# Optimization experiments

Measured on AMD Instinct MI355X. Metric: run time of the kernel, lower is better.

Reference implementation:

```python
import jax, jax.numpy as jnp
import numpy as np

B, T, D, H, L = 32, 512, 1024, 1024, 2


def setup_inputs() -> dict:
    key = jax.random.key(0)
    ks = jax.random.split(key, 7)
    s_in = 1.0 / np.sqrt(D)
    s_h = 1.0 / np.sqrt(H)
    return {
        "x": jax.random.normal(ks[0], (B, T, D), dtype=jnp.float32),
        # layer 0: input_size = D
        "W_ih0": jax.random.uniform(ks[1], (4 * H, D), jnp.float32, -s_in, s_in),
        "b0": jax.random.uniform(ks[2], (4 * H,), jnp.float32, -s_in, s_in),
        "W_hh0": jax.random.uniform(ks[3], (4 * H, H), jnp.float32, -s_h, s_h),
        # layer 1: input_size = H
        "W_ih1": jax.random.uniform(ks[4], (4 * H, H), jnp.float32, -s_h, s_h),
        "b1": jax.random.uniform(ks[5], (4 * H,), jnp.float32, -s_h, s_h),
        "W_hh1": jax.random.uniform(ks[6], (4 * H, H), jnp.float32, -s_h, s_h),
    }


def _lstm_layer(x_seq, W_ih, b, W_hh):
    # x_seq: [T, B, Din]. Precompute the input-to-gate GEMM for all steps
    # (mathematically identical to per-step, but one big GEMM).
    gx = jnp.einsum('tbd,gd->tbg', x_seq, W_ih) + b  # [T, B, 4H]
    h0 = jnp.zeros((x_seq.shape[1], W_hh.shape[1]), x_seq.dtype)
    c0 = jnp.zeros_like(h0)

    def step(carry, gx_t):
        h, c = carry
        gates = gx_t + h @ W_hh.T  # [B, 4H]
        i, f, g, o = jnp.split(gates, 4, axis=-1)  # torch chunk order: i,f,g,o
        i = jax.nn.sigmoid(i)
        f = jax.nn.sigmoid(f)
        g = jnp.tanh(g)
        o = jax.nn.sigmoid(o)
        c_new = f * c + i * g
        h_new = o * jnp.tanh(c_new)
        return (h_new, c_new), h_new

    (h_n, c_n), hs = jax.lax.scan(step, (h0, c0), gx)
    return hs, h_n, c_n  # hs: [T, B, H]


def reference(x, W_ih0, b0, W_hh0, W_ih1, b1, W_hh1):
    xs = jnp.transpose(x, (1, 0, 2))  # batch_first -> [T, B, D]
    hs0, h0_n, c0_n = _lstm_layer(xs, W_ih0, b0, W_hh0)
    hs1, h1_n, c1_n = _lstm_layer(hs0, W_ih1, b1, W_hh1)
    output = jnp.transpose(hs1, (1, 0, 2))  # [B, T, H]
    h_n = jnp.stack([h0_n, h1_n], axis=0)  # [L, B, H]
    c_n = jnp.stack([c0_n, c1_n], axis=0)
    return output, (h_n, c_n)
```

## Files before the change

### kernel.cpp

```cpp
#include <hip/hip_runtime.h>
#include <stdint.h>

typedef __attribute__((ext_vector_type(8))) short short8;
typedef __attribute__((ext_vector_type(4))) short short4v;
typedef __attribute__((ext_vector_type(4))) float f32x4;
typedef __attribute__((ext_vector_type(4))) unsigned int u32x4;
typedef __attribute__((ext_vector_type(4))) int i32x4;
typedef __attribute__((ext_vector_type(2))) unsigned long long u64x2;

__device__ inline unsigned short f2bf(float f) {
  unsigned int u = __builtin_bit_cast(unsigned int, f);
  u += 0x7fffu + ((u >> 16) & 1u);
  return (unsigned short)(u >> 16);
}
__device__ inline float bf2f(unsigned short s) {
  return __builtin_bit_cast(float, (unsigned int)s << 16);
}

__device__ inline unsigned long long stale64(unsigned long long v) {
  unsigned long long x = v ^ 0x7f7f7f7f7f7f7f7full;
  return (x - 0x0001000100010001ull) & ~x & 0x8000800080008000ull;
}


__global__ __launch_bounds__(256) void cvt_x_kernel(const float* __restrict__ x,
                                                    short* __restrict__ xbf) {
  const int total = (16384 * 1024) / 4;
  for (int i = blockIdx.x * blockDim.x + threadIdx.x; i < total;
       i += gridDim.x * blockDim.x) {
    int d4 = i & 255;
    int m  = i >> 8;
    int t = m >> 5, b = m & 31;
    float4 v = *(const float4*)(x + ((size_t)b * 512 + t) * 1024 + (size_t)d4 * 4);
    short4v o;
    o.x = (short)f2bf(v.x); o.y = (short)f2bf(v.y);
    o.z = (short)f2bf(v.z); o.w = (short)f2bf(v.w);
    *(short4v*)(xbf + (size_t)m * 1024 + d4 * 4) = o;
  }
}

__global__ __launch_bounds__(256) void cvt_w_kernel(const float* __restrict__ W,
                                                    short* __restrict__ Wp) {
  const int total = (4096 * 1024) / 4;
  for (int i = blockIdx.x * blockDim.x + threadIdx.x; i < total;
       i += gridDim.x * blockDim.x) {
    int k4 = i & 255;
    int n  = i >> 8;
    int g = n & 3, j = n >> 2;
    float4 v = *(const float4*)(W + ((size_t)g * 1024 + j) * 1024 + (size_t)k4 * 4);
    short4v o;
    o.x = (short)f2bf(v.x); o.y = (short)f2bf(v.y);
    o.z = (short)f2bf(v.z); o.w = (short)f2bf(v.w);
    *(short4v*)(Wp + (size_t)n * 1024 + k4 * 4) = o;
  }
}

__global__ __launch_bounds__(256) void cvt_b_kernel(const float* __restrict__ b,
                                                    float* __restrict__ bp) {
  int n = blockIdx.x * blockDim.x + threadIdx.x;
  if (n < 4096) bp[n] = b[(n & 3) * 1024 + (n >> 2)];
}

__global__ __launch_bounds__(256) void gemm_bt(const short* __restrict__ A,
                                               const short* __restrict__ Bm,
                                               short* __restrict__ C) {
  const int n0 = blockIdx.x * 128;
  const int m0 = blockIdx.y * 128;
  const int tid = threadIdx.x;
  const int lane = tid & 63, wid = tid >> 6;
  const int wr = wid >> 1, wc = wid & 1;
  const int fr = lane & 15, fq = lane >> 4;

  __shared__ __align__(16) short As[128 * 32];
  __shared__ __align__(16) short Bs[128 * 32];

  f32x4 acc[4][4];
#pragma unroll
  for (int i = 0; i < 4; i++)
#pragma unroll
    for (int j = 0; j < 4; j++) acc[i][j] = (f32x4){0.f, 0.f, 0.f, 0.f};

  for (int kt = 0; kt < 1024; kt += 32) {
#pragma unroll
    for (int s = 0; s < 2; s++) {
      int c = tid + s * 256;
      int row = c >> 2;
      int off = (c & 3) * 8;
      *(u32x4*)&As[row * 32 + off] =
          *(const u32x4*)(A + (size_t)(n0 + row) * 1024 + kt + off);
      *(u32x4*)&Bs[row * 32 + off] =
          *(const u32x4*)(Bm + (size_t)(m0 + row) * 1024 + kt + off);
    }
    __syncthreads();
    short8 af[4], bf[4];
#pragma unroll
    for (int i = 0; i < 4; i++)
      af[i] = *(const short8*)&As[(wr * 64 + i * 16 + fr) * 32 + fq * 8];
#pragma unroll
    for (int j = 0; j < 4; j++)
      bf[j] = *(const short8*)&Bs[(wc * 64 + j * 16 + fr) * 32 + fq * 8];
#pragma unroll
    for (int i = 0; i < 4; i++)
#pragma unroll
      for (int j = 0; j < 4; j++)
        acc[i][j] = __builtin_amdgcn_mfma_f32_16x16x32_bf16(af[i], bf[j], acc[i][j], 0, 0, 0);
    __syncthreads();
  }

#pragma unroll
  for (int i = 0; i < 4; i++) {
#pragma unroll
    for (int j = 0; j < 4; j++) {
      int nq = n0 + wr * 64 + i * 16 + fq * 4;
      int m = m0 + wc * 64 + j * 16 + fr;
      int t = m >> 5, b = m & 31;
      unsigned long long pk = 0;
#pragma unroll
      for (int r = 0; r < 4; r++)
        pk |= (unsigned long long)f2bf(acc[i][j][r]) << (16 * r);
      *(unsigned long long*)&C[(size_t)t * 131072 + (size_t)b * 4096 + nq] = pk;
    }
  }
}

#define POLL8(HBP)                                                            \
  do {                                                                        \
    i32x4 r0, r1, r2, r3, r4, r5, r6, r7;                                     \
    while (true) {                                                            \
      asm volatile(                                                           \
          "global_load_dwordx4 %0, %8, %16 sc0 sc1\n\t"                       \
          "global_load_dwordx4 %1, %9, %16 sc0 sc1\n\t"                       \
          "global_load_dwordx4 %2, %10, %16 sc0 sc1\n\t"                      \
          "global_load_dwordx4 %3, %11, %16 sc0 sc1\n\t"                      \
          "global_load_dwordx4 %4, %12, %16 sc0 sc1\n\t"                      \
          "global_load_dwordx4 %5, %13, %16 sc0 sc1\n\t"                      \
          "global_load_dwordx4 %6, %14, %16 sc0 sc1\n\t"                      \
          "global_load_dwordx4 %7, %15, %16 sc0 sc1\n\t"                      \
          "s_waitcnt vmcnt(0)"                                                \
          : "=&v"(r0), "=&v"(r1), "=&v"(r2), "=&v"(r3), "=&v"(r4),            \
            "=&v"(r5), "=&v"(r6), "=&v"(r7)                                   \
          : "v"(soff[0]), "v"(soff[1]), "v"(soff[2]), "v"(soff[3]),           \
            "v"(soff[4]), "v"(soff[5]), "v"(soff[6]), "v"(soff[7]),           \
            "s"(HBP)                                                          \
          : "memory");                                                        \
      u64x2 q0 = __builtin_bit_cast(u64x2, r0), q1 = __builtin_bit_cast(u64x2, r1); \
      u64x2 q2 = __builtin_bit_cast(u64x2, r2), q3 = __builtin_bit_cast(u64x2, r3); \
      u64x2 q4 = __builtin_bit_cast(u64x2, r4), q5 = __builtin_bit_cast(u64x2, r5); \
      u64x2 q6 = __builtin_bit_cast(u64x2, r6), q7 = __builtin_bit_cast(u64x2, r7); \
      unsigned long long bad =                                                \
          stale64(q0.x) | stale64(q0.y) | stale64(q1.x) | stale64(q1.y) |     \
          stale64(q2.x) | stale64(q2.y) | stale64(q3.x) | stale64(q3.y) |     \
          stale64(q4.x) | stale64(q4.y) | stale64(q5.x) | stale64(q5.y) |     \
          stale64(q6.x) | stale64(q6.y) | stale64(q7.x) | stale64(q7.y);      \
      if (!bad) break;                                                        \
    }                                                                         \
    *(i32x4*)&img[widx[0]] = r0;                                              \
    *(i32x4*)&img[widx[1]] = r1;                                              \
    *(i32x4*)&img[widx[2]] = r2;                                              \
    *(i32x4*)&img[widx[3]] = r3;                                              \
    *(i32x4*)&img[widx[4]] = r4;                                              \
    *(i32x4*)&img[widx[5]] = r5;                                              \
    *(i32x4*)&img[widx[6]] = r6;                                              \
    *(i32x4*)&img[widx[7]] = r7;                                              \
  } while (0)

__global__ __launch_bounds__(512, 1) void lstm_fused(
    const short* __restrict__ gx0, const short* __restrict__ whh0,
    const float* __restrict__ b0p, const short* __restrict__ wih1,
    const short* __restrict__ whh1, const float* __restrict__ b1p,
    short* __restrict__ hs0, short* __restrict__ hs1,
    float* __restrict__ out, float* __restrict__ hn, float* __restrict__ cn) {
  const int tid = threadIdx.x;
  const int lane = tid & 63, w = tid >> 6;
  const int fr = lane & 15, fq = lane >> 4;

  __shared__ __align__(16) short img[32 * 1024];
  __shared__ __align__(16) float red[4 * 64 * 4];

  if (blockIdx.x < 64) {
    const int rg = (int)blockIdx.x >> 1, bg = (int)blockIdx.x & 1;
    const int n_base = rg * 128 + w * 16;
    const int b = bg * 16 + fr;
    const int jb = rg * 32 + w * 4;
    const int j = jb + fq;
    const int sw = fr & 7;

    const short* arow = whh0 + (size_t)(n_base + fr) * 1024 + fq * 8;
    short8 wreg[32];
#pragma unroll
    for (int kk = 0; kk < 32; kk++) wreg[kk] = *(const short8*)(arow + kk * 32);

    float bia[4];
#pragma unroll
    for (int r = 0; r < 4; r++) bia[r] = b0p[n_base + fq * 4 + r];

    unsigned int soff[4];
    int widx[4];
#pragma unroll
    for (int i = 0; i < 4; i++) {
      int ch = tid + i * 512;
      soff[i] = (unsigned int)ch * 16;
      int bb = ch >> 7, cc = ch & 127;
      widx[i] = bb * 1024 + ((cc ^ (bb & 7)) << 3);
    }

    float cell = 0.f;
    for (int t = 0; t < 512; ++t) {
      unsigned long long gq = *(const unsigned long long*)(
          gx0 + (size_t)t * 131072 + (size_t)b * 4096 + n_base + fq * 4);

      if (t > 0) {
        const short* hbp = hs0 + (size_t)(t - 1) * 32768 + bg * 16384;
        i32x4 r0, r1, r2, r3;
        while (true) {
          asm volatile(
              "global_load_dwordx4 %0, %4, %8 sc0 sc1\n\t"
              "global_load_dwordx4 %1, %5, %8 sc0 sc1\n\t"
              "global_load_dwordx4 %2, %6, %8 sc0 sc1\n\t"
              "global_load_dwordx4 %3, %7, %8 sc0 sc1\n\t"
              "s_waitcnt vmcnt(0)"
              : "=&v"(r0), "=&v"(r1), "=&v"(r2), "=&v"(r3)
              : "v"(soff[0]), "v"(soff[1]), "v"(soff[2]), "v"(soff[3]),
                "s"(hbp)
              : "memory");
          u64x2 q0 = __builtin_bit_cast(u64x2, r0);
          u64x2 q1 = __builtin_bit_cast(u64x2, r1);
          u64x2 q2 = __builtin_bit_cast(u64x2, r2);
          u64x2 q3 = __builtin_bit_cast(u64x2, r3);
          unsigned long long bad =
              stale64(q0.x) | stale64(q0.y) | stale64(q1.x) | stale64(q1.y) |
              stale64(q2.x) | stale64(q2.y) | stale64(q3.x) | stale64(q3.y);
          if (!bad) break;
        }
        *(i32x4*)&img[widx[0]] = r0;
        *(i32x4*)&img[widx[1]] = r1;
        *(i32x4*)&img[widx[2]] = r2;
        *(i32x4*)&img[widx[3]] = r3;
      }
      __syncthreads();

      f32x4 a0 = (f32x4){0.f,0.f,0.f,0.f}, a1 = (f32x4){0.f,0.f,0.f,0.f};
      f32x4 a2 = (f32x4){0.f,0.f,0.f,0.f}, a3 = (f32x4){0.f,0.f,0.f,0.f};
      if (t > 0) {
#pragma unroll
        for (int m = 0; m < 8; m++) {
          const int chb = fq + m * 16;
          short8 bv0 = *(const short8*)&img[fr * 1024 + (((chb + 0) ^ sw) << 3)];
          short8 bv1 = *(const short8*)&img[fr * 1024 + (((chb + 4) ^ sw) << 3)];
          short8 bv2 = *(const short8*)&img[fr * 1024 + (((chb + 8) ^ sw) << 3)];
          short8 bv3 = *(const short8*)&img[fr * 1024 + (((chb + 12) ^ sw) << 3)];
          a0 = __builtin_amdgcn_mfma_f32_16x16x32_bf16(wreg[4 * m + 0], bv0, a0, 0, 0, 0);
          a1 = __builtin_amdgcn_mfma_f32_16x16x32_bf16(wreg[4 * m + 1], bv1, a1, 0, 0, 0);
          a2 = __builtin_amdgcn_mfma_f32_16x16x32_bf16(wreg[4 * m + 2], bv2, a2, 0, 0, 0);
          a3 = __builtin_amdgcn_mfma_f32_16x16x32_bf16(wreg[4 * m + 3], bv3, a3, 0, 0, 0);
        }
      }

      float pre0 = (a0[0] + a1[0]) + (a2[0] + a3[0]) + bf2f((unsigned short)(gq & 0xFFFF)) + bia[0];
      float pre1 = (a0[1] + a1[1]) + (a2[1] + a3[1]) + bf2f((unsigned short)((gq >> 16) & 0xFFFF)) + bia[1];
      float pre2 = (a0[2] + a1[2]) + (a2[2] + a3[2]) + bf2f((unsigned short)((gq >> 32) & 0xFFFF)) + bia[2];
      float pre3 = (a0[3] + a1[3]) + (a2[3] + a3[3]) + bf2f((unsigned short)((gq >> 48) & 0xFFFF)) + bia[3];

      float iv = 1.f / (1.f + __expf(-pre0));
      float fv = 1.f / (1.f + __expf(-pre1));
      float gv = 2.f / (1.f + __expf(-2.f * pre2)) - 1.f;
      float ov = 1.f / (1.f + __expf(-pre3));
      cell = fv * cell + iv * gv;
      float h = ov * (2.f / (1.f + __expf(-2.f * cell)) - 1.f);

      unsigned int hu = (unsigned int)f2bf(h);
      unsigned int v1 = __shfl(hu, fr + 16);
      unsigned int v2 = __shfl(hu, fr + 32);
      unsigned int v3 = __shfl(hu, fr + 48);
      if (fq == 0) {
        unsigned long long pk = (unsigned long long)hu |
                                ((unsigned long long)v1 << 16) |
                                ((unsigned long long)v2 << 32) |
                                ((unsigned long long)v3 << 48);
        __hip_atomic_store(
            (unsigned long long*)(hs0 + (size_t)t * 32768 + (size_t)b * 1024 + jb),
            pk, __ATOMIC_RELAXED, __HIP_MEMORY_SCOPE_AGENT);
      }
      if (t == 511) {
        hn[b * 1024 + j] = h;
        cn[b * 1024 + j] = cell;
        break;
      }
      __syncthreads();
    }
  } else {
    const int idx = (int)blockIdx.x - 64;
    const int rg = idx >> 1, bg = idx & 1;
    const int wn = w & 3, mw = w >> 2;
    const int n_base = rg * 64 + wn * 16;
    const int b = bg * 16 + fr;
    const int jb = rg * 16 + wn * 4;
    const int j = jb + fq;
    const int sw = fr & 7;
    const int ib = mw << 14;

    const short* wsrc = mw ? wih1 : whh1;
    const short* arow = wsrc + (size_t)(n_base + fr) * 1024 + fq * 8;
    short8 wreg[32];
#pragma unroll
    for (int kk = 0; kk < 32; kk++) wreg[kk] = *(const short8*)(arow + kk * 32);

    float bia[4];
#pragma unroll
    for (int r = 0; r < 4; r++) bia[r] = b1p[n_base + fq * 4 + r];

    const int lt = tid & 255;
    unsigned int soff[8];
    int widx[8];
#pragma unroll
    for (int i = 0; i < 8; i++) {
      int ch = lt + i * 256;
      soff[i] = (unsigned int)ch * 16;
      int bb = ch >> 7, cc = ch & 127;
      widx[i] = ib + bb * 1024 + ((cc ^ (bb & 7)) << 3);
    }

    float cell = 0.f;
    for (int t = 0; t < 512; ++t) {
      if (mw) {
        const short* hbp = hs0 + (size_t)t * 32768 + bg * 16384;
        POLL8(hbp);
      } else if (t > 0) {
        const short* hbp = hs1 + (size_t)(t - 1) * 32768 + bg * 16384;
        POLL8(hbp);
      }
      __syncthreads();

      f32x4 a0 = (f32x4){0.f,0.f,0.f,0.f}, a1 = (f32x4){0.f,0.f,0.f,0.f};
      f32x4 a2 = (f32x4){0.f,0.f,0.f,0.f}, a3 = (f32x4){0.f,0.f,0.f,0.f};
      if (mw || t > 0) {
#pragma unroll
        for (int m = 0; m < 8; m++) {
          const int chb = fq + m * 16;
          short8 bv0 = *(const short8*)&img[ib + fr * 1024 + (((chb + 0) ^ sw) << 3)];
          short8 bv1 = *(const short8*)&img[ib + fr * 1024 + (((chb + 4) ^ sw) << 3)];
          short8 bv2 = *(const short8*)&img[ib + fr * 1024 + (((chb + 8) ^ sw) << 3)];
          short8 bv3 = *(const short8*)&img[ib + fr * 1024 + (((chb + 12) ^ sw) << 3)];
          a0 = __builtin_amdgcn_mfma_f32_16x16x32_bf16(wreg[4 * m + 0], bv0, a0, 0, 0, 0);
          a1 = __builtin_amdgcn_mfma_f32_16x16x32_bf16(wreg[4 * m + 1], bv1, a1, 0, 0, 0);
          a2 = __builtin_amdgcn_mfma_f32_16x16x32_bf16(wreg[4 * m + 2], bv2, a2, 0, 0, 0);
          a3 = __builtin_amdgcn_mfma_f32_16x16x32_bf16(wreg[4 * m + 3], bv3, a3, 0, 0, 0);
        }
      }
      f32x4 s4 = (a0 + a1) + (a2 + a3);
      if (mw) *(f32x4*)&red[(wn * 64 + lane) * 4] = s4;
      __syncthreads();

      if (!mw) {
        const f32x4 o4 = *(const f32x4*)&red[(wn * 64 + lane) * 4];
        float pre0 = s4[0] + o4[0] + bia[0];
        float pre1 = s4[1] + o4[1] + bia[1];
        float pre2 = s4[2] + o4[2] + bia[2];
        float pre3 = s4[3] + o4[3] + bia[3];

        float iv = 1.f / (1.f + __expf(-pre0));
        float fv = 1.f / (1.f + __expf(-pre1));
        float gv = 2.f / (1.f + __expf(-2.f * pre2)) - 1.f;
        float ov = 1.f / (1.f + __expf(-pre3));
        cell = fv * cell + iv * gv;
        float h = ov * (2.f / (1.f + __expf(-2.f * cell)) - 1.f);

        unsigned int hu = (unsigned int)f2bf(h);
        unsigned int v1 = __shfl(hu, fr + 16);
        unsigned int v2 = __shfl(hu, fr + 32);
        unsigned int v3 = __shfl(hu, fr + 48);
        if (fq == 0) {
          unsigned long long pk = (unsigned long long)hu |
                                  ((unsigned long long)v1 << 16) |
                                  ((unsigned long long)v2 << 32) |
                                  ((unsigned long long)v3 << 48);
          __hip_atomic_store(
              (unsigned long long*)(hs1 + (size_t)t * 32768 + (size_t)b * 1024 + jb),
              pk, __ATOMIC_RELAXED, __HIP_MEMORY_SCOPE_AGENT);
        }
        out[(size_t)b * 524288 + (size_t)t * 1024 + j] = h;
        if (t == 511) {
          hn[32768 + b * 1024 + j] = h;
          cn[32768 + b * 1024 + j] = cell;
        }
      }
      if (t == 511) break;
      __syncthreads();
    }
  }
}

extern "C" void kernel_launch(void* const* d_in, const int* in_sizes, int n_in,
                              void* d_out, int out_size, void* d_ws, size_t ws_size,
                              hipStream_t stream) {
  const float* x    = (const float*)d_in[0];
  const float* Wih0 = (const float*)d_in[1];
  const float* b0   = (const float*)d_in[2];
  const float* Whh0 = (const float*)d_in[3];
  const float* Wih1 = (const float*)d_in[4];
  const float* b1   = (const float*)d_in[5];
  const float* Whh1 = (const float*)d_in[6];

  float* out = (float*)d_out;
  float* hn  = out + 16777216;
  float* cn  = hn + 65536;

  char* ws = (char*)d_ws;
  size_t off = 0;
  auto carve = [&](size_t bytes) {
    char* p = ws + off;
    off += (bytes + 255) & ~(size_t)255;
    return p;
  };
  short* xbf   = (short*)carve(16384ull * 1024 * 2);
  short* wih0p = (short*)carve(4096ull * 1024 * 2);
  short* whh0p = (short*)carve(4096ull * 1024 * 2);
  short* wih1p = (short*)carve(4096ull * 1024 * 2);
  short* whh1p = (short*)carve(4096ull * 1024 * 2);
  float* b0p   = (float*)carve(4096 * 4);
  float* b1p   = (float*)carve(4096 * 4);
  short* gx    = (short*)carve(512ull * 4096 * 32 * 2);
  short* hs0   = (short*)carve(16384ull * 1024 * 2);

  hipLaunchKernelGGL(cvt_x_kernel, dim3(4096), dim3(256), 0, stream, x, xbf);
  hipLaunchKernelGGL(cvt_w_kernel, dim3(1024), dim3(256), 0, stream, Wih0, wih0p);
  hipLaunchKernelGGL(cvt_w_kernel, dim3(1024), dim3(256), 0, stream, Whh0, whh0p);
  hipLaunchKernelGGL(cvt_w_kernel, dim3(1024), dim3(256), 0, stream, Wih1, wih1p);
  hipLaunchKernelGGL(cvt_w_kernel, dim3(1024), dim3(256), 0, stream, Whh1, whh1p);
  hipLaunchKernelGGL(cvt_b_kernel, dim3(16), dim3(256), 0, stream, b0, b0p);
  hipLaunchKernelGGL(cvt_b_kernel, dim3(16), dim3(256), 0, stream, b1, b1p);
  hipMemsetAsync(hs0, 0x7F, 16384ull * 1024 * 2, stream);

  hipLaunchKernelGGL(gemm_bt, dim3(32, 128), dim3(256), 0, stream, wih0p, xbf, gx);

  short* hs1 = xbf;
  hipMemsetAsync(hs1, 0x7F, 16384ull * 1024 * 2, stream);

  hipLaunchKernelGGL(lstm_fused, dim3(192), dim3(512), 0, stream,
                     (const short*)gx, (const short*)whh0p, (const float*)b0p,
                     (const short*)wih1p, (const short*)whh1p, (const float*)b1p,
                     hs0, hs1, out, hn, cn);
}
```

Before: 2.119 ms.

## Replace sentinel polling on hidden states with per-step block flags

Producer blocks now drain their stores, barrier, and set a per-timestep per-block flag. Consumers spin on that small flag array before doing a single load of the hidden-state slice, instead of repeatedly reloading the whole slice and checking for 0x7F sentinel values. This removes the two large sentinel memsets and the repeated full-slice polling traffic. The cost is an extra vmcnt drain and barrier on each step, plus one more memory round trip for the flag. The gx loads and output stores also become nontemporal.

```diff
diff --git a/kernel.cpp b/kernel.cpp
--- a/kernel.cpp
+++ b/kernel.cpp
@@ -6,7 +6,6 @@
 typedef __attribute__((ext_vector_type(4))) float f32x4;
 typedef __attribute__((ext_vector_type(4))) unsigned int u32x4;
 typedef __attribute__((ext_vector_type(4))) int i32x4;
-typedef __attribute__((ext_vector_type(2))) unsigned long long u64x2;
 
 __device__ inline unsigned short f2bf(float f) {
   unsigned int u = __builtin_bit_cast(unsigned int, f);
@@ -15,11 +14,6 @@
 }
 __device__ inline float bf2f(unsigned short s) {
   return __builtin_bit_cast(float, (unsigned int)s << 16);
-}
-
-__device__ inline unsigned long long stale64(unsigned long long v) {
-  unsigned long long x = v ^ 0x7f7f7f7f7f7f7f7full;
-  return (x - 0x0001000100010001ull) & ~x & 0x8000800080008000ull;
 }
 
 
@@ -123,37 +117,25 @@
   }
 }
 
-#define POLL8(HBP)                                                            \
+#define LOAD8(HBP)                                                            \
   do {                                                                        \
     i32x4 r0, r1, r2, r3, r4, r5, r6, r7;                                     \
-    while (true) {                                                            \
-      asm volatile(                                                           \
-          "global_load_dwordx4 %0, %8, %16 sc0 sc1\n\t"                       \
-          "global_load_dwordx4 %1, %9, %16 sc0 sc1\n\t"                       \
-          "global_load_dwordx4 %2, %10, %16 sc0 sc1\n\t"                      \
-          "global_load_dwordx4 %3, %11, %16 sc0 sc1\n\t"                      \
-          "global_load_dwordx4 %4, %12, %16 sc0 sc1\n\t"                      \
-          "global_load_dwordx4 %5, %13, %16 sc0 sc1\n\t"                      \
-          "global_load_dwordx4 %6, %14, %16 sc0 sc1\n\t"                      \
-          "global_load_dwordx4 %7, %15, %16 sc0 sc1\n\t"                      \
-          "s_waitcnt vmcnt(0)"                                                \
-          : "=&v"(r0), "=&v"(r1), "=&v"(r2), "=&v"(r3), "=&v"(r4),            \
-            "=&v"(r5), "=&v"(r6), "=&v"(r7)                                   \
-          : "v"(soff[0]), "v"(soff[1]), "v"(soff[2]), "v"(soff[3]),           \
-            "v"(soff[4]), "v"(soff[5]), "v"(soff[6]), "v"(soff[7]),           \
-            "s"(HBP)                                                          \
-          : "memory");                                                        \
-      u64x2 q0 = __builtin_bit_cast(u64x2, r0), q1 = __builtin_bit_cast(u64x2, r1); \
-      u64x2 q2 = __builtin_bit_cast(u64x2, r2), q3 = __builtin_bit_cast(u64x2, r3); \
-      u64x2 q4 = __builtin_bit_cast(u64x2, r4), q5 = __builtin_bit_cast(u64x2, r5); \
-      u64x2 q6 = __builtin_bit_cast(u64x2, r6), q7 = __builtin_bit_cast(u64x2, r7); \
-      unsigned long long bad =                                                \
-          stale64(q0.x) | stale64(q0.y) | stale64(q1.x) | stale64(q1.y) |     \
-          stale64(q2.x) | stale64(q2.y) | stale64(q3.x) | stale64(q3.y) |     \
-          stale64(q4.x) | stale64(q4.y) | stale64(q5.x) | stale64(q5.y) |     \
-          stale64(q6.x) | stale64(q6.y) | stale64(q7.x) | stale64(q7.y);      \
-      if (!bad) break;                                                        \
-    }                                                                         \
+    asm volatile(                                                             \
+        "global_load_dwordx4 %0, %8, %16 sc0 sc1\n\t"                         \
+        "global_load_dwordx4 %1, %9, %16 sc0 sc1\n\t"                         \
+        "global_load_dwordx4 %2, %10, %16 sc0 sc1\n\t"                        \
+        "global_load_dwordx4 %3, %11, %16 sc0 sc1\n\t"                        \
+        "global_load_dwordx4 %4, %12, %16 sc0 sc1\n\t"                        \
+        "global_load_dwordx4 %5, %13, %16 sc0 sc1\n\t"                        \
+        "global_load_dwordx4 %6, %14, %16 sc0 sc1\n\t"                        \
+        "global_load_dwordx4 %7, %15, %16 sc0 sc1\n\t"                        \
+        "s_waitcnt vmcnt(0)"                                                  \
+        : "=&v"(r0), "=&v"(r1), "=&v"(r2), "=&v"(r3), "=&v"(r4),              \
+          "=&v"(r5), "=&v"(r6), "=&v"(r7)                                     \
+        : "v"(soff[0]), "v"(soff[1]), "v"(soff[2]), "v"(soff[3]),             \
+          "v"(soff[4]), "v"(soff[5]), "v"(soff[6]), "v"(soff[7]),             \
+          "s"(HBP)                                                            \
+        : "memory");                                                          \
     *(i32x4*)&img[widx[0]] = r0;                                              \
     *(i32x4*)&img[widx[1]] = r1;                                              \
     *(i32x4*)&img[widx[2]] = r2;                                              \
@@ -164,11 +146,22 @@
     *(i32x4*)&img[widx[7]] = r7;                                              \
   } while (0)
 
+#define FLAGWAIT(FBASE, FOFF)                                                 \
+  do {                                                                        \
+    unsigned int fv_;                                                         \
+    do {                                                                      \
+      asm volatile("global_load_dword %0, %1, %2 sc0 sc1\n\t"                 \
+                   "s_waitcnt vmcnt(0)"                                       \
+                   : "=v"(fv_) : "v"(FOFF), "s"(FBASE) : "memory");           \
+    } while (!__all(fv_ != 0));                                               \
+  } while (0)
+
 __global__ __launch_bounds__(512, 1) void lstm_fused(
     const short* __restrict__ gx0, const short* __restrict__ whh0,
     const float* __restrict__ b0p, const short* __restrict__ wih1,
     const short* __restrict__ whh1, const float* __restrict__ b1p,
     short* __restrict__ hs0, short* __restrict__ hs1,
+    unsigned int* __restrict__ flags0, unsigned int* __restrict__ flags1,
     float* __restrict__ out, float* __restrict__ hn, float* __restrict__ cn) {
   const int tid = threadIdx.x;
   const int lane = tid & 63, w = tid >> 6;
@@ -203,35 +196,29 @@
       int bb = ch >> 7, cc = ch & 127;
       widx[i] = bb * 1024 + ((cc ^ (bb & 7)) << 3);
     }
+    const unsigned int foff = (unsigned int)((lane & 31) << 2);
 
     float cell = 0.f;
     for (int t = 0; t < 512; ++t) {
-      unsigned long long gq = *(const unsigned long long*)(
-          gx0 + (size_t)t * 131072 + (size_t)b * 4096 + n_base + fq * 4);
+      unsigned long long gq = __builtin_nontemporal_load(
+          (const unsigned long long*)(gx0 + (size_t)t * 131072 +
+                                      (size_t)b * 4096 + n_base + fq * 4));
 
       if (t > 0) {
+        const unsigned int* fb = flags0 + ((size_t)(t - 1) * 2 + bg) * 32;
+        FLAGWAIT(fb, foff);
         const short* hbp = hs0 + (size_t)(t - 1) * 32768 + bg * 16384;
         i32x4 r0, r1, r2, r3;
-        while (true) {
-          asm volatile(
-              "global_load_dwordx4 %0, %4, %8 sc0 sc1\n\t"
-              "global_load_dwordx4 %1, %5, %8 sc0 sc1\n\t"
-              "global_load_dwordx4 %2, %6, %8 sc0 sc1\n\t"
-              "global_load_dwordx4 %3, %7, %8 sc0 sc1\n\t"
-              "s_waitcnt vmcnt(0)"
-              : "=&v"(r0), "=&v"(r1), "=&v"(r2), "=&v"(r3)
-              : "v"(soff[0]), "v"(soff[1]), "v"(soff[2]), "v"(soff[3]),
-                "s"(hbp)
-              : "memory");
-          u64x2 q0 = __builtin_bit_cast(u64x2, r0);
-          u64x2 q1 = __builtin_bit_cast(u64x2, r1);
-          u64x2 q2 = __builtin_bit_cast(u64x2, r2);
-          u64x2 q3 = __builtin_bit_cast(u64x2, r3);
-          unsigned long long bad =
-              stale64(q0.x) | stale64(q0.y) | stale64(q1.x) | stale64(q1.y) |
-              stale64(q2.x) | stale64(q2.y) | stale64(q3.x) | stale64(q3.y);
-          if (!bad) break;
-        }
+        asm volatile(
+            "global_load_dwordx4 %0, %4, %8 sc0 sc1\n\t"
+            "global_load_dwordx4 %1, %5, %8 sc0 sc1\n\t"
+            "global_load_dwordx4 %2, %6, %8 sc0 sc1\n\t"
+            "global_load_dwordx4 %3, %7, %8 sc0 sc1\n\t"
+            "s_waitcnt vmcnt(0)"
+            : "=&v"(r0), "=&v"(r1), "=&v"(r2), "=&v"(r3)
+            : "v"(soff[0]), "v"(soff[1]), "v"(soff[2]), "v"(soff[3]),
+              "s"(hbp)
+            : "memory");
         *(i32x4*)&img[widx[0]] = r0;
         *(i32x4*)&img[widx[1]] = r1;
         *(i32x4*)&img[widx[2]] = r2;
@@ -277,16 +264,23 @@
                                 ((unsigned long long)v1 << 16) |
                                 ((unsigned long long)v2 << 32) |
                                 ((unsigned long long)v3 << 48);
-        __hip_atomic_store(
-            (unsigned long long*)(hs0 + (size_t)t * 32768 + (size_t)b * 1024 + jb),
-            pk, __ATOMIC_RELAXED, __HIP_MEMORY_SCOPE_AGENT);
+        const short* sb = hs0 + (size_t)t * 32768;
+        unsigned int voff = (unsigned int)((b * 1024 + jb) * 2);
+        asm volatile("global_store_dwordx2 %0, %1, %2 sc0 sc1"
+                     :: "v"(voff), "v"(pk), "s"(sb) : "memory");
       }
       if (t == 511) {
         hn[b * 1024 + j] = h;
         cn[b * 1024 + j] = cell;
-        break;
-      }
+      }
+      asm volatile("s_waitcnt vmcnt(0)" ::: "memory");
       __syncthreads();
+      if (tid == 0) {
+        const unsigned int* fs = flags0 + ((size_t)t * 2 + bg) * 32 + rg;
+        asm volatile("global_store_dword %0, %1, %2 sc0 sc1"
+                     :: "v"(0u), "v"(1u), "s"(fs) : "memory");
+      }
+      if (t == 511) break;
     }
   } else {
     const int idx = (int)blockIdx.x - 64;
@@ -319,15 +313,21 @@
       int bb = ch >> 7, cc = ch & 127;
       widx[i] = ib + bb * 1024 + ((cc ^ (bb & 7)) << 3);
     }
+    const unsigned int foff0 = (unsigned int)((lane & 31) << 2);
+    const unsigned int foff1 = (unsigned int)(lane << 2);
 
     float cell = 0.f;
     for (int t = 0; t < 512; ++t) {
       if (mw) {
+        const unsigned int* fb = flags0 + ((size_t)t * 2 + bg) * 32;
+        FLAGWAIT(fb, foff0);
         const short* hbp = hs0 + (size_t)t * 32768 + bg * 16384;
-        POLL8(hbp);
+        LOAD8(hbp);
       } else if (t > 0) {
+        const unsigned int* fb = flags1 + ((size_t)(t - 1) * 2 + bg) * 64;
+        FLAGWAIT(fb, foff1);
         const short* hbp = hs1 + (size_t)(t - 1) * 32768 + bg * 16384;
-        POLL8(hbp);
+        LOAD8(hbp);
       }
       __syncthreads();
 
@@ -374,18 +374,25 @@
                                   ((unsigned long long)v1 << 16) |
                                   ((unsigned long long)v2 << 32) |
                                   ((unsigned long long)v3 << 48);
-          __hip_atomic_store(
-              (unsigned long long*)(hs1 + (size_t)t * 32768 + (size_t)b * 1024 + jb),
-              pk, __ATOMIC_RELAXED, __HIP_MEMORY_SCOPE_AGENT);
+          const short* sb = hs1 + (size_t)t * 32768;
+          unsigned int voff = (unsigned int)((b * 1024 + jb) * 2);
+          asm volatile("global_store_dwordx2 %0, %1, %2 sc0 sc1"
+                       :: "v"(voff), "v"(pk), "s"(sb) : "memory");
         }
-        out[(size_t)b * 524288 + (size_t)t * 1024 + j] = h;
+        __builtin_nontemporal_store(h, &out[(size_t)b * 524288 + (size_t)t * 1024 + j]);
         if (t == 511) {
           hn[32768 + b * 1024 + j] = h;
           cn[32768 + b * 1024 + j] = cell;
         }
       }
+      asm volatile("s_waitcnt vmcnt(0)" ::: "memory");
+      __syncthreads();
+      if (tid == 0) {
+        const unsigned int* fs = flags1 + ((size_t)t * 2 + bg) * 64 + rg;
+        asm volatile("global_store_dword %0, %1, %2 sc0 sc1"
+                     :: "v"(0u), "v"(1u), "s"(fs) : "memory");
+      }
       if (t == 511) break;
-      __syncthreads();
     }
   }
 }
@@ -421,6 +428,8 @@
   float* b1p   = (float*)carve(4096 * 4);
   short* gx    = (short*)carve(512ull * 4096 * 32 * 2);
   short* hs0   = (short*)carve(16384ull * 1024 * 2);
+  unsigned int* flags0 = (unsigned int*)carve(512ull * 2 * 32 * 4);
+  unsigned int* flags1 = (unsigned int*)carve(512ull * 2 * 64 * 4);
 
   hipLaunchKernelGGL(cvt_x_kernel, dim3(4096), dim3(256), 0, stream, x, xbf);
   hipLaunchKernelGGL(cvt_w_kernel, dim3(1024), dim3(256), 0, stream, Wih0, wih0p);
@@ -429,15 +438,15 @@
   hipLaunchKernelGGL(cvt_w_kernel, dim3(1024), dim3(256), 0, stream, Whh1, whh1p);
   hipLaunchKernelGGL(cvt_b_kernel, dim3(16), dim3(256), 0, stream, b0, b0p);
   hipLaunchKernelGGL(cvt_b_kernel, dim3(16), dim3(256), 0, stream, b1, b1p);
-  hipMemsetAsync(hs0, 0x7F, 16384ull * 1024 * 2, stream);
+  hipMemsetAsync(flags0, 0, 512ull * 2 * 32 * 4, stream);
+  hipMemsetAsync(flags1, 0, 512ull * 2 * 64 * 4, stream);
 
   hipLaunchKernelGGL(gemm_bt, dim3(32, 128), dim3(256), 0, stream, wih0p, xbf, gx);
 
   short* hs1 = xbf;
-  hipMemsetAsync(hs1, 0x7F, 16384ull * 1024 * 2, stream);
 
   hipLaunchKernelGGL(lstm_fused, dim3(192), dim3(512), 0, stream,
                      (const short*)gx, (const short*)whh0p, (const float*)b0p,
                      (const short*)wih1p, (const short*)whh1p, (const float*)b1p,
-                     hs0, hs1, out, hn, cn);
-}
+                     hs0, hs1, flags0, flags1, out, hn, cn);
+}
```

Measured after the change: 3.125 ms. 1.47x slower.

## Double-buffer LDS images to drop trailing barrier and store h per-lane

Applied to the files above, without the earlier changes.

Double-buffers the shared h image and the reduction buffer by step parity, which lets the trailing __syncthreads per timestep be removed from both layer loops. The shuffle-packed 64-bit atomic store of h is replaced by per-lane 16-bit stores with sc0 sc1, and when a poll finds stale data it spins on cheaper dwordx2 loads before reloading the full dwordx4 set. The gx0 loads and output stores become nontemporal. The narrower stores mean more store transactions, and the stale-sentinel check now has to hold across separately written 16-bit values.

```diff
diff --git a/kernel.cpp b/kernel.cpp
--- a/kernel.cpp
+++ b/kernel.cpp
@@ -123,7 +123,7 @@
   }
 }
 
-#define POLL8(HBP)                                                            \
+#define PULL8_VERIFY(HBP)                                                     \
   do {                                                                        \
     i32x4 r0, r1, r2, r3, r4, r5, r6, r7;                                     \
     while (true) {                                                            \
@@ -153,15 +153,35 @@
           stale64(q4.x) | stale64(q4.y) | stale64(q5.x) | stale64(q5.y) |     \
           stale64(q6.x) | stale64(q6.y) | stale64(q7.x) | stale64(q7.y);      \
       if (!bad) break;                                                        \
+      unsigned long long p0, p1, p2, p3, p4, p5, p6, p7;                      \
+      do {                                                                    \
+        asm volatile(                                                         \
+            "global_load_dwordx2 %0, %8, %16 sc0 sc1\n\t"                     \
+            "global_load_dwordx2 %1, %9, %16 sc0 sc1\n\t"                     \
+            "global_load_dwordx2 %2, %10, %16 sc0 sc1\n\t"                    \
+            "global_load_dwordx2 %3, %11, %16 sc0 sc1\n\t"                    \
+            "global_load_dwordx2 %4, %12, %16 sc0 sc1\n\t"                    \
+            "global_load_dwordx2 %5, %13, %16 sc0 sc1\n\t"                    \
+            "global_load_dwordx2 %6, %14, %16 sc0 sc1\n\t"                    \
+            "global_load_dwordx2 %7, %15, %16 sc0 sc1\n\t"                    \
+            "s_waitcnt vmcnt(0)"                                              \
+            : "=&v"(p0), "=&v"(p1), "=&v"(p2), "=&v"(p3), "=&v"(p4),          \
+              "=&v"(p5), "=&v"(p6), "=&v"(p7)                                 \
+            : "v"(soff[0]), "v"(soff[1]), "v"(soff[2]), "v"(soff[3]),         \
+              "v"(soff[4]), "v"(soff[5]), "v"(soff[6]), "v"(soff[7]),         \
+              "s"(HBP)                                                        \
+            : "memory");                                                      \
+      } while (stale64(p0) | stale64(p1) | stale64(p2) | stale64(p3) |        \
+               stale64(p4) | stale64(p5) | stale64(p6) | stale64(p7));        \
     }                                                                         \
-    *(i32x4*)&img[widx[0]] = r0;                                              \
-    *(i32x4*)&img[widx[1]] = r1;                                              \
-    *(i32x4*)&img[widx[2]] = r2;                                              \
-    *(i32x4*)&img[widx[3]] = r3;                                              \
-    *(i32x4*)&img[widx[4]] = r4;                                              \
-    *(i32x4*)&img[widx[5]] = r5;                                              \
-    *(i32x4*)&img[widx[6]] = r6;                                              \
-    *(i32x4*)&img[widx[7]] = r7;                                              \
+    *(i32x4*)&ibw[widx[0]] = r0;                                              \
+    *(i32x4*)&ibw[widx[1]] = r1;                                              \
+    *(i32x4*)&ibw[widx[2]] = r2;                                              \
+    *(i32x4*)&ibw[widx[3]] = r3;                                              \
+    *(i32x4*)&ibw[widx[4]] = r4;                                              \
+    *(i32x4*)&ibw[widx[5]] = r5;                                              \
+    *(i32x4*)&ibw[widx[6]] = r6;                                              \
+    *(i32x4*)&ibw[widx[7]] = r7;                                              \
   } while (0)
 
 __global__ __launch_bounds__(512, 1) void lstm_fused(
@@ -174,15 +194,14 @@
   const int lane = tid & 63, w = tid >> 6;
   const int fr = lane & 15, fq = lane >> 4;
 
-  __shared__ __align__(16) short img[32 * 1024];
-  __shared__ __align__(16) float red[4 * 64 * 4];
+  __shared__ __align__(16) short img[2][32768];
+  __shared__ __align__(16) float red[2][1024];
 
   if (blockIdx.x < 64) {
     const int rg = (int)blockIdx.x >> 1, bg = (int)blockIdx.x & 1;
     const int n_base = rg * 128 + w * 16;
     const int b = bg * 16 + fr;
-    const int jb = rg * 32 + w * 4;
-    const int j = jb + fq;
+    const int j = rg * 32 + w * 4 + fq;
     const int sw = fr & 7;
 
     const short* arow = whh0 + (size_t)(n_base + fr) * 1024 + fq * 8;
@@ -206,11 +225,13 @@
 
     float cell = 0.f;
     for (int t = 0; t < 512; ++t) {
-      unsigned long long gq = *(const unsigned long long*)(
-          gx0 + (size_t)t * 131072 + (size_t)b * 4096 + n_base + fq * 4);
+      unsigned long long gq = __builtin_nontemporal_load(
+          (const unsigned long long*)(gx0 + (size_t)t * 131072 +
+                                      (size_t)b * 4096 + n_base + fq * 4));
 
       if (t > 0) {
         const short* hbp = hs0 + (size_t)(t - 1) * 32768 + bg * 16384;
+        short* ibw = img[t & 1];
         i32x4 r0, r1, r2, r3;
         while (true) {
           asm volatile(
@@ -231,24 +252,38 @@
               stale64(q0.x) | stale64(q0.y) | stale64(q1.x) | stale64(q1.y) |
               stale64(q2.x) | stale64(q2.y) | stale64(q3.x) | stale64(q3.y);
           if (!bad) break;
+          unsigned long long p0, p1, p2, p3;
+          do {
+            asm volatile(
+                "global_load_dwordx2 %0, %4, %8 sc0 sc1\n\t"
+                "global_load_dwordx2 %1, %5, %8 sc0 sc1\n\t"
+                "global_load_dwordx2 %2, %6, %8 sc0 sc1\n\t"
+                "global_load_dwordx2 %3, %7, %8 sc0 sc1\n\t"
+                "s_waitcnt vmcnt(0)"
+                : "=&v"(p0), "=&v"(p1), "=&v"(p2), "=&v"(p3)
+                : "v"(soff[0]), "v"(soff[1]), "v"(soff[2]), "v"(soff[3]),
+                  "s"(hbp)
+                : "memory");
+          } while (stale64(p0) | stale64(p1) | stale64(p2) | stale64(p3));
         }
-        *(i32x4*)&img[widx[0]] = r0;
-        *(i32x4*)&img[widx[1]] = r1;
-        *(i32x4*)&img[widx[2]] = r2;
-        *(i32x4*)&img[widx[3]] = r3;
+        *(i32x4*)&ibw[widx[0]] = r0;
+        *(i32x4*)&ibw[widx[1]] = r1;
+        *(i32x4*)&ibw[widx[2]] = r2;
+        *(i32x4*)&ibw[widx[3]] = r3;
       }
       __syncthreads();
 
       f32x4 a0 = (f32x4){0.f,0.f,0.f,0.f}, a1 = (f32x4){0.f,0.f,0.f,0.f};
       f32x4 a2 = (f32x4){0.f,0.f,0.f,0.f}, a3 = (f32x4){0.f,0.f,0.f,0.f};
       if (t > 0) {
+        const short* ibr = img[t & 1];
 #pragma unroll
         for (int m = 0; m < 8; m++) {
           const int chb = fq + m * 16;
-          short8 bv0 = *(const short8*)&img[fr * 1024 + (((chb + 0) ^ sw) << 3)];
-          short8 bv1 = *(const short8*)&img[fr * 1024 + (((chb + 4) ^ sw) << 3)];
-          short8 bv2 = *(const short8*)&img[fr * 1024 + (((chb + 8) ^ sw) << 3)];
-          short8 bv3 = *(const short8*)&img[fr * 1024 + (((chb + 12) ^ sw) << 3)];
+          short8 bv0 = *(const short8*)&ibr[fr * 1024 + (((chb + 0) ^ sw) << 3)];
+          short8 bv1 = *(const short8*)&ibr[fr * 1024 + (((chb + 4) ^ sw) << 3)];
+          short8 bv2 = *(const short8*)&ibr[fr * 1024 + (((chb + 8) ^ sw) << 3)];
+          short8 bv3 = *(const short8*)&ibr[fr * 1024 + (((chb + 12) ^ sw) << 3)];
           a0 = __builtin_amdgcn_mfma_f32_16x16x32_bf16(wreg[4 * m + 0], bv0, a0, 0, 0, 0);
           a1 = __builtin_amdgcn_mfma_f32_16x16x32_bf16(wreg[4 * m + 1], bv1, a1, 0, 0, 0);
           a2 = __builtin_amdgcn_mfma_f32_16x16x32_bf16(wreg[4 * m + 2], bv2, a2, 0, 0, 0);
@@ -268,25 +303,17 @@
       cell = fv * cell + iv * gv;
       float h = ov * (2.f / (1.f + __expf(-2.f * cell)) - 1.f);
 
-      unsigned int hu = (unsigned int)f2bf(h);
-      unsigned int v1 = __shfl(hu, fr + 16);
-      unsigned int v2 = __shfl(hu, fr + 32);
-      unsigned int v3 = __shfl(hu, fr + 48);
-      if (fq == 0) {
-        unsigned long long pk = (unsigned long long)hu |
-                                ((unsigned long long)v1 << 16) |
-                                ((unsigned long long)v2 << 32) |
-                                ((unsigned long long)v3 << 48);
-        __hip_atomic_store(
-            (unsigned long long*)(hs0 + (size_t)t * 32768 + (size_t)b * 1024 + jb),
-            pk, __ATOMIC_RELAXED, __HIP_MEMORY_SCOPE_AGENT);
+      {
+        const short* sb = hs0 + (size_t)t * 32768;
+        unsigned int voff = (unsigned int)((b * 1024 + j) * 2);
+        unsigned int hv = (unsigned int)f2bf(h);
+        asm volatile("global_store_short %0, %1, %2 sc0 sc1"
+                     :: "v"(voff), "v"(hv), "s"(sb) : "memory");
       }
       if (t == 511) {
         hn[b * 1024 + j] = h;
         cn[b * 1024 + j] = cell;
-        break;
-      }
-      __syncthreads();
+      }
     }
   } else {
     const int idx = (int)blockIdx.x - 64;
@@ -294,8 +321,7 @@
     const int wn = w & 3, mw = w >> 2;
     const int n_base = rg * 64 + wn * 16;
     const int b = bg * 16 + fr;
-    const int jb = rg * 16 + wn * 4;
-    const int j = jb + fq;
+    const int j = rg * 16 + wn * 4 + fq;
     const int sw = fr & 7;
     const int ib = mw << 14;
 
@@ -322,25 +348,27 @@
 
     float cell = 0.f;
     for (int t = 0; t < 512; ++t) {
+      short* ibw = img[t & 1];
       if (mw) {
         const short* hbp = hs0 + (size_t)t * 32768 + bg * 16384;
-        POLL8(hbp);
+        PULL8_VERIFY(hbp);
       } else if (t > 0) {
         const short* hbp = hs1 + (size_t)(t - 1) * 32768 + bg * 16384;
-        POLL8(hbp);
+        PULL8_VERIFY(hbp);
       }
       __syncthreads();
 
       f32x4 a0 = (f32x4){0.f,0.f,0.f,0.f}, a1 = (f32x4){0.f,0.f,0.f,0.f};
       f32x4 a2 = (f32x4){0.f,0.f,0.f,0.f}, a3 = (f32x4){0.f,0.f,0.f,0.f};
       if (mw || t > 0) {
+        const short* ibr = img[t & 1];
 #pragma unroll
         for (int m = 0; m < 8; m++) {
           const int chb = fq + m * 16;
-          short8 bv0 = *(const short8*)&img[ib + fr * 1024 + (((chb + 0) ^ sw) << 3)];
-          short8 bv1 = *(const short8*)&img[ib + fr * 1024 + (((chb + 4) ^ sw) << 3)];
-          short8 bv2 = *(const short8*)&img[ib + fr * 1024 + (((chb + 8) ^ sw) << 3)];
-          short8 bv3 = *(const short8*)&img[ib + fr * 1024 + (((chb + 12) ^ sw) << 3)];
+          short8 bv0 = *(const short8*)&ibr[ib + fr * 1024 + (((chb + 0) ^ sw) << 3)];
+          short8 bv1 = *(const short8*)&ibr[ib + fr * 1024 + (((chb + 4) ^ sw) << 3)];
+          short8 bv2 = *(const short8*)&ibr[ib + fr * 1024 + (((chb + 8) ^ sw) << 3)];
+          short8 bv3 = *(const short8*)&ibr[ib + fr * 1024 + (((chb + 12) ^ sw) << 3)];
           a0 = __builtin_amdgcn_mfma_f32_16x16x32_bf16(wreg[4 * m + 0], bv0, a0, 0, 0, 0);
           a1 = __builtin_amdgcn_mfma_f32_16x16x32_bf16(wreg[4 * m + 1], bv1, a1, 0, 0, 0);
           a2 = __builtin_amdgcn_mfma_f32_16x16x32_bf16(wreg[4 * m + 2], bv2, a2, 0, 0, 0);
@@ -348,11 +376,11 @@
         }
       }
       f32x4 s4 = (a0 + a1) + (a2 + a3);
-      if (mw) *(f32x4*)&red[(wn * 64 + lane) * 4] = s4;
+      if (mw) *(f32x4*)&red[t & 1][(wn * 64 + lane) * 4] = s4;
       __syncthreads();
 
       if (!mw) {
-        const f32x4 o4 = *(const f32x4*)&red[(wn * 64 + lane) * 4];
+        const f32x4 o4 = *(const f32x4*)&red[t & 1][(wn * 64 + lane) * 4];
         float pre0 = s4[0] + o4[0] + bia[0];
         float pre1 = s4[1] + o4[1] + bia[1];
         float pre2 = s4[2] + o4[2] + bia[2];
@@ -365,27 +393,19 @@
         cell = fv * cell + iv * gv;
         float h = ov * (2.f / (1.f + __expf(-2.f * cell)) - 1.f);
 
-        unsigned int hu = (unsigned int)f2bf(h);
-        unsigned int v1 = __shfl(hu, fr + 16);
-        unsigned int v2 = __shfl(hu, fr + 32);
-        unsigned int v3 = __shfl(hu, fr + 48);
-        if (fq == 0) {
-          unsigned long long pk = (unsigned long long)hu |
-                                  ((unsigned long long)v1 << 16) |
-                                  ((unsigned long long)v2 << 32) |
-                                  ((unsigned long long)v3 << 48);
-          __hip_atomic_store(
-              (unsigned long long*)(hs1 + (size_t)t * 32768 + (size_t)b * 1024 + jb),
-              pk, __ATOMIC_RELAXED, __HIP_MEMORY_SCOPE_AGENT);
+        {
+          const short* sb = hs1 + (size_t)t * 32768;
+          unsigned int voff = (unsigned int)((b * 1024 + j) * 2);
+          unsigned int hv = (unsigned int)f2bf(h);
+          asm volatile("global_store_short %0, %1, %2 sc0 sc1"
+                       :: "v"(voff), "v"(hv), "s"(sb) : "memory");
         }
-        out[(size_t)b * 524288 + (size_t)t * 1024 + j] = h;
+        __builtin_nontemporal_store(h, &out[(size_t)b * 524288 + (size_t)t * 1024 + j]);
         if (t == 511) {
           hn[32768 + b * 1024 + j] = h;
           cn[32768 + b * 1024 + j] = cell;
         }
       }
-      if (t == 511) break;
-      __syncthreads();
     }
   }
 }
```

After: 4.306 ms. +103.2%, slower.

## Double-buffer LDS h-image to drop per-step barrier in LSTM recurrence

Applied to the files above, without the earlier changes.

Turns the shared h-image and reduction buffers into two buffers indexed by step parity, so the trailing __syncthreads at the end of each timestep can be removed in both layer loops. Adds s_sleep backoff inside the stale-data polling loops to ease memory traffic while spinning. Switches the gx0 load and the output store to nontemporal hints. The cost is twice the LDS footprint, and the sleep may add wake-up latency on the critical recurrence path.

```diff
diff --git a/kernel.cpp b/kernel.cpp
--- a/kernel.cpp
+++ b/kernel.cpp
@@ -123,7 +123,7 @@
   }
 }
 
-#define POLL8(HBP)                                                            \
+#define PULL8_SPIN(HBP)                                                       \
   do {                                                                        \
     i32x4 r0, r1, r2, r3, r4, r5, r6, r7;                                     \
     while (true) {                                                            \
@@ -153,15 +153,16 @@
           stale64(q4.x) | stale64(q4.y) | stale64(q5.x) | stale64(q5.y) |     \
           stale64(q6.x) | stale64(q6.y) | stale64(q7.x) | stale64(q7.y);      \
       if (!bad) break;                                                        \
+      __builtin_amdgcn_s_sleep(2);                                            \
     }                                                                         \
-    *(i32x4*)&img[widx[0]] = r0;                                              \
-    *(i32x4*)&img[widx[1]] = r1;                                              \
-    *(i32x4*)&img[widx[2]] = r2;                                              \
-    *(i32x4*)&img[widx[3]] = r3;                                              \
-    *(i32x4*)&img[widx[4]] = r4;                                              \
-    *(i32x4*)&img[widx[5]] = r5;                                              \
-    *(i32x4*)&img[widx[6]] = r6;                                              \
-    *(i32x4*)&img[widx[7]] = r7;                                              \
+    *(i32x4*)&ibw[widx[0]] = r0;                                              \
+    *(i32x4*)&ibw[widx[1]] = r1;                                              \
+    *(i32x4*)&ibw[widx[2]] = r2;                                              \
+    *(i32x4*)&ibw[widx[3]] = r3;                                              \
+    *(i32x4*)&ibw[widx[4]] = r4;                                              \
+    *(i32x4*)&ibw[widx[5]] = r5;                                              \
+    *(i32x4*)&ibw[widx[6]] = r6;                                              \
+    *(i32x4*)&ibw[widx[7]] = r7;                                              \
   } while (0)
 
 __global__ __launch_bounds__(512, 1) void lstm_fused(
@@ -174,8 +175,8 @@
   const int lane = tid & 63, w = tid >> 6;
   const int fr = lane & 15, fq = lane >> 4;
 
-  __shared__ __align__(16) short img[32 * 1024];
-  __shared__ __align__(16) float red[4 * 64 * 4];
+  __shared__ __align__(16) short img[2][32768];
+  __shared__ __align__(16) float red[2][1024];
 
   if (blockIdx.x < 64) {
     const int rg = (int)blockIdx.x >> 1, bg = (int)blockIdx.x & 1;
@@ -206,11 +207,13 @@
 
     float cell = 0.f;
     for (int t = 0; t < 512; ++t) {
-      unsigned long long gq = *(const unsigned long long*)(
-          gx0 + (size_t)t * 131072 + (size_t)b * 4096 + n_base + fq * 4);
+      unsigned long long gq = __builtin_nontemporal_load(
+          (const unsigned long long*)(gx0 + (size_t)t * 131072 +
+                                      (size_t)b * 4096 + n_base + fq * 4));
 
       if (t > 0) {
         const short* hbp = hs0 + (size_t)(t - 1) * 32768 + bg * 16384;
+        short* ibw = img[t & 1];
         i32x4 r0, r1, r2, r3;
         while (true) {
           asm volatile(
@@ -231,24 +234,26 @@
               stale64(q0.x) | stale64(q0.y) | stale64(q1.x) | stale64(q1.y) |
               stale64(q2.x) | stale64(q2.y) | stale64(q3.x) | stale64(q3.y);
           if (!bad) break;
+          __builtin_amdgcn_s_sleep(2);
         }
-        *(i32x4*)&img[widx[0]] = r0;
-        *(i32x4*)&img[widx[1]] = r1;
-        *(i32x4*)&img[widx[2]] = r2;
-        *(i32x4*)&img[widx[3]] = r3;
+        *(i32x4*)&ibw[widx[0]] = r0;
+        *(i32x4*)&ibw[widx[1]] = r1;
+        *(i32x4*)&ibw[widx[2]] = r2;
+        *(i32x4*)&ibw[widx[3]] = r3;
       }
       __syncthreads();
 
       f32x4 a0 = (f32x4){0.f,0.f,0.f,0.f}, a1 = (f32x4){0.f,0.f,0.f,0.f};
       f32x4 a2 = (f32x4){0.f,0.f,0.f,0.f}, a3 = (f32x4){0.f,0.f,0.f,0.f};
       if (t > 0) {
+        const short* ibr = img[t & 1];
 #pragma unroll
         for (int m = 0; m < 8; m++) {
           const int chb = fq + m * 16;
-          short8 bv0 = *(const short8*)&img[fr * 1024 + (((chb + 0) ^ sw) << 3)];
-          short8 bv1 = *(const short8*)&img[fr * 1024 + (((chb + 4) ^ sw) << 3)];
-          short8 bv2 = *(const short8*)&img[fr * 1024 + (((chb + 8) ^ sw) << 3)];
-          short8 bv3 = *(const short8*)&img[fr * 1024 + (((chb + 12) ^ sw) << 3)];
+          short8 bv0 = *(const short8*)&ibr[fr * 1024 + (((chb + 0) ^ sw) << 3)];
+          short8 bv1 = *(const short8*)&ibr[fr * 1024 + (((chb + 4) ^ sw) << 3)];
+          short8 bv2 = *(const short8*)&ibr[fr * 1024 + (((chb + 8) ^ sw) << 3)];
+          short8 bv3 = *(const short8*)&ibr[fr * 1024 + (((chb + 12) ^ sw) << 3)];
           a0 = __builtin_amdgcn_mfma_f32_16x16x32_bf16(wreg[4 * m + 0], bv0, a0, 0, 0, 0);
           a1 = __builtin_amdgcn_mfma_f32_16x16x32_bf16(wreg[4 * m + 1], bv1, a1, 0, 0, 0);
           a2 = __builtin_amdgcn_mfma_f32_16x16x32_bf16(wreg[4 * m + 2], bv2, a2, 0, 0, 0);
@@ -284,9 +289,7 @@
       if (t == 511) {
         hn[b * 1024 + j] = h;
         cn[b * 1024 + j] = cell;
-        break;
-      }
-      __syncthreads();
+      }
     }
   } else {
     const int idx = (int)blockIdx.x - 64;
@@ -322,25 +325,27 @@
 
     float cell = 0.f;
     for (int t = 0; t < 512; ++t) {
+      short* ibw = img[t & 1];
       if (mw) {
         const short* hbp = hs0 + (size_t)t * 32768 + bg * 16384;
-        POLL8(hbp);
+        PULL8_SPIN(hbp);
       } else if (t > 0) {
         const short* hbp = hs1 + (size_t)(t - 1) * 32768 + bg * 16384;
-        POLL8(hbp);
+        PULL8_SPIN(hbp);
       }
       __syncthreads();
 
       f32x4 a0 = (f32x4){0.f,0.f,0.f,0.f}, a1 = (f32x4){0.f,0.f,0.f,0.f};
       f32x4 a2 = (f32x4){0.f,0.f,0.f,0.f}, a3 = (f32x4){0.f,0.f,0.f,0.f};
       if (mw || t > 0) {
+        const short* ibr = img[t & 1];
 #pragma unroll
         for (int m = 0; m < 8; m++) {
           const int chb = fq + m * 16;
-          short8 bv0 = *(const short8*)&img[ib + fr * 1024 + (((chb + 0) ^ sw) << 3)];
-          short8 bv1 = *(const short8*)&img[ib + fr * 1024 + (((chb + 4) ^ sw) << 3)];
-          short8 bv2 = *(const short8*)&img[ib + fr * 1024 + (((chb + 8) ^ sw) << 3)];
-          short8 bv3 = *(const short8*)&img[ib + fr * 1024 + (((chb + 12) ^ sw) << 3)];
+          short8 bv0 = *(const short8*)&ibr[ib + fr * 1024 + (((chb + 0) ^ sw) << 3)];
+          short8 bv1 = *(const short8*)&ibr[ib + fr * 1024 + (((chb + 4) ^ sw) << 3)];
+          short8 bv2 = *(const short8*)&ibr[ib + fr * 1024 + (((chb + 8) ^ sw) << 3)];
+          short8 bv3 = *(const short8*)&ibr[ib + fr * 1024 + (((chb + 12) ^ sw) << 3)];
           a0 = __builtin_amdgcn_mfma_f32_16x16x32_bf16(wreg[4 * m + 0], bv0, a0, 0, 0, 0);
           a1 = __builtin_amdgcn_mfma_f32_16x16x32_bf16(wreg[4 * m + 1], bv1, a1, 0, 0, 0);
           a2 = __builtin_amdgcn_mfma_f32_16x16x32_bf16(wreg[4 * m + 2], bv2, a2, 0, 0, 0);
@@ -348,11 +353,11 @@
         }
       }
       f32x4 s4 = (a0 + a1) + (a2 + a3);
-      if (mw) *(f32x4*)&red[(wn * 64 + lane) * 4] = s4;
+      if (mw) *(f32x4*)&red[t & 1][(wn * 64 + lane) * 4] = s4;
       __syncthreads();
 
       if (!mw) {
-        const f32x4 o4 = *(const f32x4*)&red[(wn * 64 + lane) * 4];
+        const f32x4 o4 = *(const f32x4*)&red[t & 1][(wn * 64 + lane) * 4];
         float pre0 = s4[0] + o4[0] + bia[0];
         float pre1 = s4[1] + o4[1] + bia[1];
         float pre2 = s4[2] + o4[2] + bia[2];
@@ -378,14 +383,12 @@
               (unsigned long long*)(hs1 + (size_t)t * 32768 + (size_t)b * 1024 + jb),
               pk, __ATOMIC_RELAXED, __HIP_MEMORY_SCOPE_AGENT);
         }
-        out[(size_t)b * 524288 + (size_t)t * 1024 + j] = h;
+        __builtin_nontemporal_store(h, &out[(size_t)b * 524288 + (size_t)t * 1024 + j]);
         if (t == 511) {
           hn[32768 + b * 1024 + j] = h;
           cn[32768 + b * 1024 + j] = cell;
         }
       }
-      if (t == 511) break;
-      __syncthreads();
     }
   }
 }
```

After: 4.141 ms. 95.4% more time.
